# Kernel tuning notes

Hardware: AMD Instinct MI355X
Metric: run time of the kernel (lower is better)

## Reference

```python
import jax, jax.numpy as jnp
import numpy as np

DIM = 256
HEADS = 4
DIM_HEAD = 64
INNER = HEADS * DIM_HEAD  # 256
SCALE = DIM_HEAD ** -0.5


def setup_inputs() -> dict:
    key = jax.random.key(0)
    k1, k2, k3 = jax.random.split(key, 3)
    x = jax.random.normal(k1, (4, 4096, DIM), dtype=jnp.float32)
    # to_qkv: Linear(dim, inner*3, bias=False) -> weight [3*inner, dim]
    w_qkv = jax.random.normal(k2, (3 * INNER, DIM), dtype=jnp.float32) * (DIM ** -0.5)
    # to_out: Linear(inner, dim) with bias
    w_out = jax.random.normal(k3, (DIM, INNER), dtype=jnp.float32) * (INNER ** -0.5)
    b_out = jnp.zeros((DIM,), dtype=jnp.float32)
    return {"x": x, "w_qkv": w_qkv, "w_out": w_out, "b_out": b_out}


def reference(x, w_qkv, w_out, b_out):
    b, n, _ = x.shape
    qkv = x @ w_qkv.T                      # [b, n, 3*inner]
    q, k, v = jnp.split(qkv, 3, axis=-1)   # each [b, n, inner]

    def heads(t):
        return t.reshape(b, n, HEADS, DIM_HEAD).transpose(0, 2, 1, 3)  # [b, h, n, d]

    q, k, v = heads(q), heads(k), heads(v)
    dots = jnp.einsum('bhid,bhjd->bhij', q, k) * SCALE   # [b, h, n, n]
    attn = jax.nn.softmax(dots, axis=-1)
    out = jnp.einsum('bhij,bhjd->bhid', attn, v)         # [b, h, n, d]
    out = out.transpose(0, 2, 1, 3).reshape(b, n, INNER)  # [b, n, inner]
    return out @ w_out.T + b_out  # dropout p=0.0 -> identity
```

## Files before the change

kernel.cpp:

```cpp
#include <hip/hip_runtime.h>
#include <hip/hip_bf16.h>
#include <stdint.h>

typedef unsigned short ushort_t;
typedef __attribute__((ext_vector_type(8))) short short8;
typedef __attribute__((ext_vector_type(4))) ushort_t ushort4v;
typedef __attribute__((ext_vector_type(4))) float float4v;
typedef __attribute__((ext_vector_type(16))) float floatx16;

#define MFMA32(a, b, c) __builtin_amdgcn_mfma_f32_32x32x16_bf16(a, b, c, 0, 0, 0)

#define BATCH 4
#define SEQ 4096
#define DIM 256
#define HEADS 4
#define DHEAD 64
#define INNER 256
#define MROWS (BATCH * SEQ)
#define NQKV (3 * INNER)

__device__ __forceinline__ ushort_t f2bf(float f) {
    uint32_t u = __builtin_bit_cast(uint32_t, f);
    uint32_t r = (u + 0x7FFFu + ((u >> 16) & 1u)) >> 16;
    return (ushort_t)r;
}

__device__ __forceinline__ float exp2_fast(float x) {
#if __has_builtin(__builtin_amdgcn_exp2f)
    return __builtin_amdgcn_exp2f(x);
#else
    return exp2f(x);
#endif
}

__device__ __forceinline__ unsigned cvtpk_bf16(float lo, float hi) {
    unsigned r;
    asm("v_cvt_pk_bf16_f32 %0, %1, %2" : "=v"(r) : "v"(lo), "v"(hi));
    return r;
}

__device__ __forceinline__ void plswap(unsigned& a, unsigned& b) {
#if __has_builtin(__builtin_amdgcn_permlane32_swap)
    auto rr = __builtin_amdgcn_permlane32_swap(a, b, false, false);
    a = (unsigned)rr[0];
    b = (unsigned)rr[1];
#else
    unsigned sa = (unsigned)__shfl_xor((int)a, 32, 64);
    unsigned sb = (unsigned)__shfl_xor((int)b, 32, 64);
    bool upper = (threadIdx.x & 32) != 0;
    unsigned na = upper ? sb : a;
    unsigned nb = upper ? b : sa;
    a = na;
    b = nb;
#endif
}

__device__ __forceinline__ void gload_lds16(const ushort_t* g, ushort_t* l) {
    __builtin_amdgcn_global_load_lds(
        (__attribute__((address_space(1))) void*)(const_cast<ushort_t*>(g)),
        (__attribute__((address_space(3))) void*)l, 16, 0, 0);
}

__global__ __launch_bounds__(256) void convert_w(
    const float* __restrict__ wqkv, const float* __restrict__ wout,
    ushort_t* __restrict__ wqkvb, ushort_t* __restrict__ woutb) {
    const int NW = NQKV * DIM;
    const int NO = DIM * INNER;
    const float QS = 0.125f * 1.4426950408889634f;
    int idx = blockIdx.x * blockDim.x + threadIdx.x;
    int stride = gridDim.x * blockDim.x;
    for (int i = idx; i < NW + NO; i += stride) {
        if (i < NW) {
            float s = (i < INNER * DIM) ? QS : 1.0f;
            wqkvb[i] = f2bf(wqkv[i] * s);
        } else {
            int j = i - NW;
            woutb[j] = f2bf(wout[j]);
        }
    }
}

__global__ __launch_bounds__(256) void qkv_gemm(
    const float* __restrict__ X, const ushort_t* __restrict__ B,
    ushort_t* __restrict__ q, ushort_t* __restrict__ k, ushort_t* __restrict__ v) {
    __shared__ ushort_t Bs[128 * 256] __attribute__((aligned(16)));
    int bid = blockIdx.x;
    int swz = (bid & 7) * 96 + (bid >> 3);
    int mt = swz / 6, nb = swz % 6;
    int tid = threadIdx.x;
    int wid = tid >> 6, lane = tid & 63;
    const int l31 = lane & 31, hi = lane >> 5;

    const ushort_t* bsrc = B + (int64_t)nb * 128 * 256;
#pragma unroll
    for (int i = 0; i < 16; ++i) {
        int L = i * 256 + tid;
        int sl = L ^ ((L >> 5) & 31);
        gload_lds16(bsrc + (sl >> 5) * 256 + (sl & 31) * 8, &Bs[L * 8]);
    }

    int m0 = mt * 128 + wid * 32;
    const float* abase = X + (int64_t)(m0 + l31) * 256 + hi * 8;
    short8 af[16];
#pragma unroll
    for (int s = 0; s < 16; ++s) {
        float4v a0 = *(const float4v*)(abase + s * 16);
        float4v a1 = *(const float4v*)(abase + s * 16 + 4);
        union { unsigned u[4]; short8 s8; } fu;
        fu.u[0] = cvtpk_bf16(a0[0], a0[1]);
        fu.u[1] = cvtpk_bf16(a0[2], a0[3]);
        fu.u[2] = cvtpk_bf16(a1[0], a1[1]);
        fu.u[3] = cvtpk_bf16(a1[2], a1[3]);
        af[s] = fu.s8;
    }

    __syncthreads();

    floatx16 acc[4] = {};
    __builtin_amdgcn_s_setprio(1);
#pragma unroll
    for (int s = 0; s < 16; ++s) {
#pragma unroll
        for (int nt = 0; nt < 4; ++nt) {
            int n = nt * 32 + l31;
            int byte = (n * 512 + s * 32 + hi * 16) ^ ((n & 31) << 4);
            short8 bf = *(const short8*)((const char*)Bs + byte);
            acc[nt] = MFMA32(af[s], bf, acc[nt]);
        }
    }
    __builtin_amdgcn_s_setprio(0);

    int part = nb >> 1;
    if (part < 2) {
        ushort_t* dst = (part == 0) ? q : k;
#pragma unroll
        for (int nt = 0; nt < 4; ++nt) {
            int cc = (nb * 128 + nt * 32 + l31) & 255;
            int h = cc >> 6, d = cc & 63;
#pragma unroll
            for (int r = 0; r < 16; ++r) {
                int m = m0 + (r & 3) + 8 * (r >> 2) + 4 * hi;
                int bb = m >> 12, n = m & 4095;
                dst[((((int64_t)bb * HEADS + h) * SEQ) + n) * DHEAD + d] = f2bf(acc[nt][r]);
            }
        }
    } else {
#pragma unroll
        for (int nt = 0; nt < 4; ++nt) {
            int cc = (nb * 128 + nt * 32 + l31) & 255;
            int h = cc >> 6, d = cc & 63;
#pragma unroll
            for (int g = 0; g < 4; ++g) {
                int m = m0 + g * 8 + hi * 4;
                int bb = m >> 12, n = m & 4095;
                ushort4v pk;
#pragma unroll
                for (int r = 0; r < 4; ++r) pk[r] = f2bf(acc[nt][g * 4 + r]);
                *(ushort4v*)(v + ((((int64_t)bb * HEADS + h) * DHEAD) + d) * SEQ + n) = pk;
            }
        }
    }
}

__global__ __launch_bounds__(256) void attn_kernel(
    const ushort_t* __restrict__ Qg, const ushort_t* __restrict__ Kg,
    const ushort_t* __restrict__ Vtg, ushort_t* __restrict__ Og) {
    int bid = blockIdx.x;
    int swz = (bid & 7) * 64 + (bid >> 3);
    int bh = swz >> 5;
    int qt = swz & 31;
    int tid = threadIdx.x;
    int wid = tid >> 6, lane = tid & 63;
    const int l31 = lane & 31;
    const int hi = lane >> 5;

    __shared__ ushort_t SM[2][8192] __attribute__((aligned(16)));

    const ushort_t* qbase = Qg + (int64_t)bh * SEQ * DHEAD;
    const ushort_t* kbase = Kg + (int64_t)bh * SEQ * DHEAD;
    const ushort_t* vtbase = Vtg + (int64_t)bh * DHEAD * SEQ;

    int q0 = qt * 128 + wid * 32;
    short8 qf[4];
#pragma unroll
    for (int s = 0; s < 4; ++s)
        qf[s] = *(const short8*)(qbase + (int64_t)(q0 + l31) * DHEAD + s * 16 + hi * 8);

    union { ushort_t u[8]; short8 s8; } onesu;
#pragma unroll
    for (int j = 0; j < 8; ++j) onesu.u[j] = 0x3F80;
    const short8 ones8 = onesu.s8;

    const ushort_t* kp[2];
    const ushort_t* vp[2];
    ushort_t* kld[2];
    ushort_t* vld[2];
#pragma unroll
    for (int jj = 0; jj < 2; ++jj) {
        int L = jj * 256 + tid;
        int sl = L ^ ((L >> 6) & 7);
        int s_ = sl >> 7, hi_ = (sl >> 6) & 1, low = sl & 63;
        kp[jj] = kbase + (int64_t)low * DHEAD + s_ * 16 + hi_ * 8;
        vp[jj] = vtbase + (int64_t)low * SEQ + s_ * 16 + hi_ * 8;
        kld[jj] = &SM[0][(jj * 256 + wid * 64) * 8];
        vld[jj] = &SM[0][4096 + (jj * 256 + wid * 64) * 8];
    }

#define STAGE(BUF)                                          \
    {                                                       \
        _Pragma("unroll") for (int jj = 0; jj < 2; ++jj) {  \
            gload_lds16(kp[jj], kld[jj] + (BUF) * 8192);    \
            gload_lds16(vp[jj], vld[jj] + (BUF) * 8192);    \
            kp[jj] += 64 * DHEAD;                           \
            vp[jj] += 64;                                   \
        }                                                   \
    }

    int bS[4];
#pragma unroll
    for (int s = 0; s < 4; ++s) bS[s] = s * 2048 + hi * 1024 + ((l31 * 16) ^ ((s * 2 + hi) << 4));

    floatx16 accO[2] = {};
    floatx16 accL = {};

    STAGE(0);
    __syncthreads();

    for (int it = 0; it < SEQ / 64; ++it) {
        int buf = it & 1;
        const char* smc = (const char*)SM + buf * 16384;
        const char* smv = smc + 8192;
        if (it < SEQ / 64 - 1) STAGE(buf ^ 1);

#pragma unroll
        for (int kt = 0; kt < 2; ++kt) {
            floatx16 accS = {};
#pragma unroll
            for (int s = 0; s < 4; ++s) {
                short8 kf = *(const short8*)(smc + bS[s] + kt * 512);
                accS = MFMA32(kf, qf[s], accS);
            }
#pragma unroll
            for (int r = 0; r < 16; ++r) accS[r] = exp2_fast(accS[r]);

            unsigned w0 = cvtpk_bf16(accS[0], accS[1]);
            unsigned w1 = cvtpk_bf16(accS[2], accS[3]);
            unsigned w2 = cvtpk_bf16(accS[4], accS[5]);
            unsigned w3 = cvtpk_bf16(accS[6], accS[7]);
            unsigned w4 = cvtpk_bf16(accS[8], accS[9]);
            unsigned w5 = cvtpk_bf16(accS[10], accS[11]);
            unsigned w6 = cvtpk_bf16(accS[12], accS[13]);
            unsigned w7 = cvtpk_bf16(accS[14], accS[15]);
            plswap(w0, w2);
            plswap(w1, w3);
            plswap(w4, w6);
            plswap(w5, w7);
            union { unsigned u[4]; short8 s; } f0, f1;
            f0.u[0] = w0; f0.u[1] = w1; f0.u[2] = w2; f0.u[3] = w3;
            f1.u[0] = w4; f1.u[1] = w5; f1.u[2] = w6; f1.u[3] = w7;
            const short8 pa0 = f0.s;
            const short8 pa1 = f1.s;

            {
                int ks = 2 * kt;
                int va = ks * 2048 + hi * 1024 + ((l31 * 16) ^ ((ks * 2 + hi) << 4));
                short8 vf0 = *(const short8*)(smv + va);
                short8 vf1 = *(const short8*)(smv + va + 512);
                accO[0] = MFMA32(pa0, vf0, accO[0]);
                accO[1] = MFMA32(pa0, vf1, accO[1]);
                accL = MFMA32(pa0, ones8, accL);
                ks = 2 * kt + 1;
                va = ks * 2048 + hi * 1024 + ((l31 * 16) ^ ((ks * 2 + hi) << 4));
                vf0 = *(const short8*)(smv + va);
                vf1 = *(const short8*)(smv + va + 512);
                accO[0] = MFMA32(pa1, vf0, accO[0]);
                accO[1] = MFMA32(pa1, vf1, accO[1]);
                accL = MFMA32(pa1, ones8, accL);
            }
        }

        __syncthreads();
    }

    int b = bh >> 2, h = bh & 3;
#pragma unroll
    for (int r = 0; r < 16; ++r) {
        int qr = (r & 3) + 8 * (r >> 2) + 4 * hi;
        float inv = 1.f / accL[r];
        int n = q0 + qr;
#pragma unroll
        for (int o = 0; o < 2; ++o) {
            int d = o * 32 + l31;
            Og[((int64_t)b * SEQ + n) * INNER + h * 64 + d] = f2bf(accO[o][r] * inv);
        }
    }
#undef STAGE
}

__global__ __launch_bounds__(256) void proj_gemm(
    const ushort_t* __restrict__ A, const ushort_t* __restrict__ B,
    const float* __restrict__ bias, float* __restrict__ out) {
    __shared__ ushort_t Bs[128 * 256] __attribute__((aligned(16)));
    int bid = blockIdx.x;
    int swz = (bid & 7) * 64 + (bid >> 3);
    int mt = swz >> 1, nb = swz & 1;
    int tid = threadIdx.x;
    int wid = tid >> 6, lane = tid & 63;
    const int l31 = lane & 31, hi = lane >> 5;

    const ushort_t* bsrc = B + (int64_t)nb * 128 * 256;
#pragma unroll
    for (int i = 0; i < 16; ++i) {
        int L = i * 256 + tid;
        int sl = L ^ ((L >> 5) & 31);
        gload_lds16(bsrc + (sl >> 5) * 256 + (sl & 31) * 8, &Bs[L * 8]);
    }

    int m0 = mt * 64 + (wid & 1) * 32;
    int nside = wid >> 1;
    const ushort_t* abase = A + (int64_t)(m0 + l31) * 256 + hi * 8;
    short8 af[16];
#pragma unroll
    for (int s = 0; s < 16; ++s) af[s] = *(const short8*)(abase + s * 16);

    __syncthreads();

    floatx16 acc[2] = {};
    __builtin_amdgcn_s_setprio(1);
#pragma unroll
    for (int s = 0; s < 16; ++s) {
#pragma unroll
        for (int nt = 0; nt < 2; ++nt) {
            int n = nside * 64 + nt * 32 + l31;
            int byte = (n * 512 + s * 32 + hi * 16) ^ ((n & 31) << 4);
            short8 bf = *(const short8*)((const char*)Bs + byte);
            acc[nt] = MFMA32(af[s], bf, acc[nt]);
        }
    }
    __builtin_amdgcn_s_setprio(0);

#pragma unroll
    for (int nt = 0; nt < 2; ++nt) {
        int col = nb * 128 + nside * 64 + nt * 32 + l31;
        float bv = bias[col];
#pragma unroll
        for (int r = 0; r < 16; ++r) {
            int m = m0 + (r & 3) + 8 * (r >> 2) + 4 * hi;
            out[(int64_t)m * DIM + col] = acc[nt][r] + bv;
        }
    }
}

extern "C" void kernel_launch(void* const* d_in, const int* in_sizes, int n_in,
                              void* d_out, int out_size, void* d_ws, size_t ws_size,
                              hipStream_t stream) {
    const float* x = (const float*)d_in[0];
    const float* w_qkv = (const float*)d_in[1];
    const float* w_out = (const float*)d_in[2];
    const float* b_out = (const float*)d_in[3];
    float* out = (float*)d_out;

    ushort_t* ws = (ushort_t*)d_ws;
    const int64_t NW = (int64_t)NQKV * DIM;
    const int64_t NO = (int64_t)DIM * INNER;
    const int64_t NH = (int64_t)BATCH * HEADS * SEQ * DHEAD;
    ushort_t* wqkvb = ws;
    ushort_t* woutb = wqkvb + NW;
    ushort_t* qb = woutb + NO;
    ushort_t* kb = qb + NH;
    ushort_t* vb = kb + NH;
    ushort_t* ob = vb + NH;

    convert_w<<<256, 256, 0, stream>>>(w_qkv, w_out, wqkvb, woutb);
    qkv_gemm<<<768, 256, 0, stream>>>(x, wqkvb, qb, kb, vb);
    attn_kernel<<<512, 256, 0, stream>>>(qb, kb, vb, ob);
    proj_gemm<<<512, 256, 0, stream>>>(ob, woutb, b_out, out);
}
```

Baseline: 123.2 us.

## Split attention KV range across two blocks and merge partial outputs

Splits each query tile's key/value sequence into two halves handled by separate blocks, doubling the attention grid from 512 to 1024 blocks. Each block writes its unnormalized fp32 output and row sums to workspace, and a new merge kernel adds the halves, normalizes and converts to bf16. The aim is better occupancy across the GPU's compute units. In exchange it adds fp32 partial-output traffic and an extra kernel launch. The merge is valid without a max-rescale only because the softmax already uses no running max.

```diff
diff --git a/kernel.cpp b/kernel.cpp
--- a/kernel.cpp
+++ b/kernel.cpp
@@ -164,11 +164,13 @@
 
 __global__ __launch_bounds__(256) void attn_kernel(
     const ushort_t* __restrict__ Qg, const ushort_t* __restrict__ Kg,
-    const ushort_t* __restrict__ Vtg, ushort_t* __restrict__ Og) {
+    const ushort_t* __restrict__ Vtg, float* __restrict__ opart,
+    float* __restrict__ lbuf) {
     int bid = blockIdx.x;
-    int swz = (bid & 7) * 64 + (bid >> 3);
-    int bh = swz >> 5;
-    int qt = swz & 31;
+    int swz = (bid & 7) * 128 + (bid >> 3);
+    int bh = swz >> 6;
+    int qt = (swz >> 1) & 31;
+    int half = swz & 1;
     int tid = threadIdx.x;
     int wid = tid >> 6, lane = tid & 63;
     const int l31 = lane & 31;
@@ -179,6 +181,7 @@
     const ushort_t* qbase = Qg + (int64_t)bh * SEQ * DHEAD;
     const ushort_t* kbase = Kg + (int64_t)bh * SEQ * DHEAD;
     const ushort_t* vtbase = Vtg + (int64_t)bh * DHEAD * SEQ;
+    const int kv0 = half * 2048;
 
     int q0 = qt * 128 + wid * 32;
     short8 qf[4];
@@ -200,8 +203,8 @@
         int L = jj * 256 + tid;
         int sl = L ^ ((L >> 6) & 7);
         int s_ = sl >> 7, hi_ = (sl >> 6) & 1, low = sl & 63;
-        kp[jj] = kbase + (int64_t)low * DHEAD + s_ * 16 + hi_ * 8;
-        vp[jj] = vtbase + (int64_t)low * SEQ + s_ * 16 + hi_ * 8;
+        kp[jj] = kbase + (int64_t)(kv0 + low) * DHEAD + s_ * 16 + hi_ * 8;
+        vp[jj] = vtbase + (int64_t)low * SEQ + kv0 + s_ * 16 + hi_ * 8;
         kld[jj] = &SM[0][(jj * 256 + wid * 64) * 8];
         vld[jj] = &SM[0][4096 + (jj * 256 + wid * 64) * 8];
     }
@@ -226,11 +229,11 @@
     STAGE(0);
     __syncthreads();
 
-    for (int it = 0; it < SEQ / 64; ++it) {
+    for (int it = 0; it < 2048 / 64; ++it) {
         int buf = it & 1;
         const char* smc = (const char*)SM + buf * 16384;
         const char* smv = smc + 8192;
-        if (it < SEQ / 64 - 1) STAGE(buf ^ 1);
+        if (it < 2048 / 64 - 1) STAGE(buf ^ 1);
 
 #pragma unroll
         for (int kt = 0; kt < 2; ++kt) {
@@ -282,19 +285,51 @@
         __syncthreads();
     }
 
-    int b = bh >> 2, h = bh & 3;
+    float* ob2 = opart + (int64_t)(half * 16 + bh) * SEQ * 64;
 #pragma unroll
     for (int r = 0; r < 16; ++r) {
         int qr = (r & 3) + 8 * (r >> 2) + 4 * hi;
-        float inv = 1.f / accL[r];
         int n = q0 + qr;
 #pragma unroll
         for (int o = 0; o < 2; ++o) {
-            int d = o * 32 + l31;
-            Og[((int64_t)b * SEQ + n) * INNER + h * 64 + d] = f2bf(accO[o][r] * inv);
+            ob2[(int64_t)n * 64 + o * 32 + l31] = accO[o][r];
+        }
+    }
+    if (l31 == 0) {
+        float* lb = lbuf + (int64_t)(half * 16 + bh) * SEQ;
+#pragma unroll
+        for (int r = 0; r < 16; ++r) {
+            int qr = (r & 3) + 8 * (r >> 2) + 4 * hi;
+            lb[q0 + qr] = accL[r];
         }
     }
 #undef STAGE
+}
+
+__global__ __launch_bounds__(256) void merge_kernel(
+    const float* __restrict__ opart, const float* __restrict__ lbuf,
+    ushort_t* __restrict__ ob) {
+    int f = blockIdx.x * 256 + threadIdx.x;
+    int d8 = f & 7;
+    int n = (f >> 3) & 4095;
+    int bh = f >> 15;
+
+    float L = lbuf[(int64_t)bh * SEQ + n] + lbuf[(int64_t)(16 + bh) * SEQ + n];
+    float inv = 1.f / L;
+
+    const float4v* p0 = (const float4v*)(opart + ((int64_t)bh * SEQ + n) * 64 + d8 * 8);
+    const float4v* p1 = (const float4v*)(opart + ((int64_t)(16 + bh) * SEQ + n) * 64 + d8 * 8);
+    float4v a0 = p0[0], a1 = p0[1];
+    float4v b0 = p1[0], b1 = p1[1];
+
+    union { unsigned u[4]; short8 s8; } fu;
+    fu.u[0] = cvtpk_bf16((a0[0] + b0[0]) * inv, (a0[1] + b0[1]) * inv);
+    fu.u[1] = cvtpk_bf16((a0[2] + b0[2]) * inv, (a0[3] + b0[3]) * inv);
+    fu.u[2] = cvtpk_bf16((a1[0] + b1[0]) * inv, (a1[1] + b1[1]) * inv);
+    fu.u[3] = cvtpk_bf16((a1[2] + b1[2]) * inv, (a1[3] + b1[3]) * inv);
+
+    int b = bh >> 2, h = bh & 3;
+    *(short8*)(ob + ((int64_t)b * SEQ + n) * INNER + h * 64 + d8 * 8) = fu.s8;
 }
 
 __global__ __launch_bounds__(256) void proj_gemm(
@@ -370,9 +405,12 @@
     ushort_t* kb = qb + NH;
     ushort_t* vb = kb + NH;
     ushort_t* ob = vb + NH;
+    float* opart = (float*)(ob + NH);
+    float* lbuf = opart + (int64_t)2 * 16 * SEQ * 64;
 
     convert_w<<<256, 256, 0, stream>>>(w_qkv, w_out, wqkvb, woutb);
     qkv_gemm<<<768, 256, 0, stream>>>(x, wqkvb, qb, kb, vb);
-    attn_kernel<<<512, 256, 0, stream>>>(qb, kb, vb, ob);
+    attn_kernel<<<1024, 256, 0, stream>>>(qb, kb, vb, opart, lbuf);
+    merge_kernel<<<2048, 256, 0, stream>>>(opart, lbuf, ob);
     proj_gemm<<<512, 256, 0, stream>>>(ob, woutb, b_out, out);
 }
```

Result: slower. 130.7 us (+6.1%).

## Load K/V fragments directly from global memory instead of LDS double-buffering

Applied to the files above, without the earlier changes.

Removes the shared-memory double-buffered staging of K and V tiles in the attention kernel. Each wave now loads its K and V MFMA fragments straight from global memory into registers every iteration, with no barriers. This drops the LDS traffic and the __syncthreads, but the four waves in a block now each fetch the same K/V data separately (4x redundant global/L2 traffic), and nothing prefetches the next tile to hide load latency.

```diff
diff --git a/kernel.cpp b/kernel.cpp
--- a/kernel.cpp
+++ b/kernel.cpp
@@ -174,8 +174,6 @@
     const int l31 = lane & 31;
     const int hi = lane >> 5;
 
-    __shared__ ushort_t SM[2][8192] __attribute__((aligned(16)));
-
     const ushort_t* qbase = Qg + (int64_t)bh * SEQ * DHEAD;
     const ushort_t* kbase = Kg + (int64_t)bh * SEQ * DHEAD;
     const ushort_t* vtbase = Vtg + (int64_t)bh * DHEAD * SEQ;
@@ -191,55 +189,37 @@
     for (int j = 0; j < 8; ++j) onesu.u[j] = 0x3F80;
     const short8 ones8 = onesu.s8;
 
-    const ushort_t* kp[2];
-    const ushort_t* vp[2];
-    ushort_t* kld[2];
-    ushort_t* vld[2];
-#pragma unroll
-    for (int jj = 0; jj < 2; ++jj) {
-        int L = jj * 256 + tid;
-        int sl = L ^ ((L >> 6) & 7);
-        int s_ = sl >> 7, hi_ = (sl >> 6) & 1, low = sl & 63;
-        kp[jj] = kbase + (int64_t)low * DHEAD + s_ * 16 + hi_ * 8;
-        vp[jj] = vtbase + (int64_t)low * SEQ + s_ * 16 + hi_ * 8;
-        kld[jj] = &SM[0][(jj * 256 + wid * 64) * 8];
-        vld[jj] = &SM[0][4096 + (jj * 256 + wid * 64) * 8];
-    }
-
-#define STAGE(BUF)                                          \
-    {                                                       \
-        _Pragma("unroll") for (int jj = 0; jj < 2; ++jj) {  \
-            gload_lds16(kp[jj], kld[jj] + (BUF) * 8192);    \
-            gload_lds16(vp[jj], vld[jj] + (BUF) * 8192);    \
-            kp[jj] += 64 * DHEAD;                           \
-            vp[jj] += 64;                                   \
-        }                                                   \
-    }
-
-    int bS[4];
-#pragma unroll
-    for (int s = 0; s < 4; ++s) bS[s] = s * 2048 + hi * 1024 + ((l31 * 16) ^ ((s * 2 + hi) << 4));
+    const int kOff0 = l31 * 64 + hi * 8;
+    const int kOff1 = (32 + l31) * 64 + hi * 8;
+    const int vOff0 = l31 * SEQ + hi * 8;
+    const int vOff1 = (32 + l31) * SEQ + hi * 8;
+
+    const ushort_t* kT = kbase;
+    const ushort_t* vT = vtbase;
 
     floatx16 accO[2] = {};
     floatx16 accL = {};
 
-    STAGE(0);
-    __syncthreads();
-
     for (int it = 0; it < SEQ / 64; ++it) {
-        int buf = it & 1;
-        const char* smc = (const char*)SM + buf * 16384;
-        const char* smv = smc + 8192;
-        if (it < SEQ / 64 - 1) STAGE(buf ^ 1);
+        short8 kf0[4], kf1[4];
+#pragma unroll
+        for (int s = 0; s < 4; ++s) {
+            kf0[s] = *(const short8*)(kT + kOff0 + s * 16);
+            kf1[s] = *(const short8*)(kT + kOff1 + s * 16);
+        }
+        short8 vfa[4], vfb[4];
+#pragma unroll
+        for (int ks = 0; ks < 4; ++ks) {
+            vfa[ks] = *(const short8*)(vT + vOff0 + ks * 16);
+            vfb[ks] = *(const short8*)(vT + vOff1 + ks * 16);
+        }
 
 #pragma unroll
         for (int kt = 0; kt < 2; ++kt) {
             floatx16 accS = {};
 #pragma unroll
-            for (int s = 0; s < 4; ++s) {
-                short8 kf = *(const short8*)(smc + bS[s] + kt * 512);
-                accS = MFMA32(kf, qf[s], accS);
-            }
+            for (int s = 0; s < 4; ++s)
+                accS = MFMA32(kt ? kf1[s] : kf0[s], qf[s], accS);
 #pragma unroll
             for (int r = 0; r < 16; ++r) accS[r] = exp2_fast(accS[r]);
 
@@ -261,25 +241,18 @@
             const short8 pa0 = f0.s;
             const short8 pa1 = f1.s;
 
-            {
-                int ks = 2 * kt;
-                int va = ks * 2048 + hi * 1024 + ((l31 * 16) ^ ((ks * 2 + hi) << 4));
-                short8 vf0 = *(const short8*)(smv + va);
-                short8 vf1 = *(const short8*)(smv + va + 512);
-                accO[0] = MFMA32(pa0, vf0, accO[0]);
-                accO[1] = MFMA32(pa0, vf1, accO[1]);
-                accL = MFMA32(pa0, ones8, accL);
-                ks = 2 * kt + 1;
-                va = ks * 2048 + hi * 1024 + ((l31 * 16) ^ ((ks * 2 + hi) << 4));
-                vf0 = *(const short8*)(smv + va);
-                vf1 = *(const short8*)(smv + va + 512);
-                accO[0] = MFMA32(pa1, vf0, accO[0]);
-                accO[1] = MFMA32(pa1, vf1, accO[1]);
-                accL = MFMA32(pa1, ones8, accL);
-            }
-        }
-
-        __syncthreads();
+            int ks = 2 * kt;
+            accO[0] = MFMA32(pa0, vfa[ks], accO[0]);
+            accO[1] = MFMA32(pa0, vfb[ks], accO[1]);
+            accL = MFMA32(pa0, ones8, accL);
+            ks = 2 * kt + 1;
+            accO[0] = MFMA32(pa1, vfa[ks], accO[0]);
+            accO[1] = MFMA32(pa1, vfb[ks], accO[1]);
+            accL = MFMA32(pa1, ones8, accL);
+        }
+
+        kT += 64 * DHEAD;
+        vT += 64;
     }
 
     int b = bh >> 2, h = bh & 3;
@@ -294,7 +267,6 @@
             Og[((int64_t)b * SEQ + n) * INNER + h * 64 + d] = f2bf(accO[o][r] * inv);
         }
     }
-#undef STAGE
 }
 
 __global__ __launch_bounds__(256) void proj_gemm(
```

After: 269.5 us. +118.7%, slower.
